# Performance work log

Hardware: AMD Instinct MI355X
Metric: run time of the kernel (lower is better)

## Reference

```python
import jax, jax.numpy as jnp
import numpy as np

NUM_BINS = 32
SIGMA_RATIO = 1.0
SMOOTH_NR = 1e-7
SMOOTH_DR = 1e-7


def _parzen_weights(x, bin_centers, preterm):
    # x: [B, N]; returns normalized Gaussian Parzen weights [B, N, K]
    d = x[..., None] - bin_centers  # [B, N, K]
    w = jnp.exp(-preterm * d * d)
    return w / jnp.sum(w, axis=-1, keepdims=True)


def _mi_loss(pred, target):
    B = pred.shape[0]
    p = pred.reshape(B, -1)  # [B, N]
    t = target.reshape(B, -1)
    N = p.shape[1]

    # min/max are detached (.item() in torch); images in [0,1] use fixed range (0,1)
    minval = jax.lax.stop_gradient(jnp.minimum(p.min(), t.min()))
    maxval = jax.lax.stop_gradient(jnp.maximum(p.max(), t.max()))
    in_range = (maxval <= 1.0) & (minval >= 0.0)
    minval = jnp.where(in_range, jnp.float32(0.0), minval)
    maxval = jnp.where(in_range, jnp.float32(1.0), maxval)

    bin_centers = minval + (maxval - minval) * jnp.linspace(0.0, 1.0, NUM_BINS, dtype=p.dtype)  # [K]
    sigma = (maxval - minval) / (NUM_BINS - 1) * SIGMA_RATIO
    preterm = 1.0 / (2.0 * sigma * sigma)

    wa = _parzen_weights(p, bin_centers, preterm)  # [B, N, K]
    wb = _parzen_weights(t, bin_centers, preterm)  # [B, N, K]

    pa = jnp.mean(wa, axis=1)  # [B, K] == pa of shape B,1,K squeezed
    pb = jnp.mean(wb, axis=1)  # [B, K]
    pab = jnp.einsum('bnk,bnl->bkl', wa, wb) / N  # [B, K, K] joint histogram
    papb = pa[:, :, None] * pb[:, None, :]  # [B, K, K] outer product == bmm(pa^T, pb)

    mi = jnp.sum(pab * jnp.log((pab + SMOOTH_NR) / (papb + SMOOTH_DR) + SMOOTH_DR), axis=(-1, -2))  # [B]
    return -jnp.mean(mi)  # reduction='mean', negated


def setup_inputs() -> dict:
    key = jax.random.key(0)
    k1, k2 = jax.random.split(key)
    shape = (1, 1, 128, 128, 128)
    pred = jax.random.uniform(k1, shape, dtype=jnp.float32)
    target = jax.random.uniform(k2, shape, dtype=jnp.float32)
    return {"pred": pred, "target": target}


def reference(pred, target):
    return _mi_loss(pred, target)
```

## Files before the change

### kernel.cpp

```cpp
#include <hip/hip_runtime.h>
#include <math.h>

#ifndef __has_builtin
#define __has_builtin(x) 0
#endif
#if __has_builtin(__builtin_amdgcn_exp2f)
#define EXP2F(x) __builtin_amdgcn_exp2f(x)
#else
#define EXP2F(x) exp2f(x)
#endif
#if __has_builtin(__builtin_amdgcn_rcpf)
#define RCPF(x) __builtin_amdgcn_rcpf(x)
#else
#define RCPF(x) (1.0f / (x))
#endif

typedef _Float16 f16x8 __attribute__((ext_vector_type(8)));
typedef _Float16 h2 __attribute__((ext_vector_type(2)));
typedef float f32x4 __attribute__((ext_vector_type(4)));

union Frag {
  f16x8 v;
  h2 p[4];
  _Float16 e[8];
};

__device__ __forceinline__ h2 pkrtz(float a, float b) {
#if __has_builtin(__builtin_amdgcn_cvt_pkrtz)
  return __builtin_bit_cast(h2, __builtin_amdgcn_cvt_pkrtz(a, b));
#else
  h2 r; r.x = (_Float16)a; r.y = (_Float16)b; return r;
#endif
}

constexpr int KBINS = 32;
constexpr int MM_BLOCKS = 512;
constexpr int MAIN_BLOCKS = 1024;
constexpr int NTHR = 512;
constexpr int WPB = 8;
constexpr int BATCH = 32;
constexpr int RED_BLOCKS = 64;
constexpr int PART_OFF_F = 4096;
constexpr size_t REDA_OFF_B = (size_t)(PART_OFF_F + MAIN_BLOCKS * KBINS * KBINS) * 4;
constexpr float WSCALE = 512.0f;

#define MFMA16(a, b, c) __builtin_amdgcn_mfma_f32_16x16x32_f16((a), (b), (c), 0, 0, 0)

template <int CTRL>
__device__ __forceinline__ float rot_add(float v) {
  int r = __builtin_amdgcn_update_dpp(0, __builtin_bit_cast(int, v), CTRL, 0xF, 0xF, true);
  return v + __builtin_bit_cast(float, r);
}
__device__ __forceinline__ float row_sum16(float v) {
  v = rot_add<0x128>(v);
  v = rot_add<0x124>(v);
  v = rot_add<0x122>(v);
  v = rot_add<0x121>(v);
  return v;
}

__device__ __forceinline__ void wpair(float x, float c0, float c1, float npl2,
                                      float& w0, float& w1) {
  float d0 = x - c0, d1 = x - c1;
  float e0 = EXP2F(fmaf(npl2 * d0, d0, 9.0f));
  float e1 = EXP2F(fmaf(npl2 * d1, d1, 9.0f));
  float s = row_sum16(e0 + e1);
  float inv = RCPF(s);
  inv = inv * fmaf(-s, inv, 2.0f);
  inv *= WSCALE;
  w0 = e0 * inv;
  w1 = e1 * inv;
}

__global__ __launch_bounds__(256) void k_minmax(const float* __restrict__ p,
                                                const float* __restrict__ t,
                                                int n, float* __restrict__ ws) {
  int tid = blockIdx.x * 256 + threadIdx.x;
  int nth = gridDim.x * 256;
  float mn = INFINITY, mx = -INFINITY;
  int n4 = n >> 2;
  const float4* p4 = (const float4*)p;
  const float4* t4 = (const float4*)t;
  for (int i = tid; i < n4; i += nth) {
    float4 a = p4[i];
    mn = fminf(mn, fminf(fminf(a.x, a.y), fminf(a.z, a.w)));
    mx = fmaxf(mx, fmaxf(fmaxf(a.x, a.y), fmaxf(a.z, a.w)));
    float4 b = t4[i];
    mn = fminf(mn, fminf(fminf(b.x, b.y), fminf(b.z, b.w)));
    mx = fmaxf(mx, fmaxf(fmaxf(b.x, b.y), fmaxf(b.z, b.w)));
  }
  for (int i = (n4 << 2) + tid; i < n; i += nth) {
    mn = fminf(mn, fminf(p[i], t[i]));
    mx = fmaxf(mx, fmaxf(p[i], t[i]));
  }
  for (int off = 32; off; off >>= 1) {
    mn = fminf(mn, __shfl_xor(mn, off, 64));
    mx = fmaxf(mx, __shfl_xor(mx, off, 64));
  }
  __shared__ float smn[4], smx[4];
  int wv = threadIdx.x >> 6;
  if ((threadIdx.x & 63) == 0) { smn[wv] = mn; smx[wv] = mx; }
  __syncthreads();
  if (threadIdx.x == 0) {
    mn = fminf(fminf(smn[0], smn[1]), fminf(smn[2], smn[3]));
    mx = fmaxf(fmaxf(smx[0], smx[1]), fmaxf(smx[2], smx[3]));
    ws[16 + 2 * blockIdx.x] = mn;
    ws[17 + 2 * blockIdx.x] = mx;
  }
}

__global__ __launch_bounds__(NTHR, 4) void k_main(const float* __restrict__ p,
                                                  const float* __restrict__ t,
                                                  int n, float* __restrict__ ws) {
  __shared__ __align__(16) float red[WPB][KBINS * KBINS];
  __shared__ float s_par[4];

  const int tidx = threadIdx.x;
  const int lane = tidx & 63;
  const int wv = tidx >> 6;

  if (tidx < 64) {
    float mn = INFINITY, mx = -INFINITY;
    for (int b = lane; b < MM_BLOCKS; b += 64) {
      mn = fminf(mn, ws[16 + 2 * b]);
      mx = fmaxf(mx, ws[17 + 2 * b]);
    }
    for (int off = 32; off; off >>= 1) {
      mn = fminf(mn, __shfl_xor(mn, off, 64));
      mx = fmaxf(mx, __shfl_xor(mx, off, 64));
    }
    if (lane == 0) {
      bool in_range = (mx <= 1.0f) && (mn >= 0.0f);
      float minv = in_range ? 0.0f : mn;
      float maxv = in_range ? 1.0f : mx;
      float drange = maxv - minv;
      float sigma = drange * (1.0f / (KBINS - 1));
      float preterm = 1.0f / (2.0f * sigma * sigma);
      s_par[0] = minv;
      s_par[1] = drange * (1.0f / (KBINS - 1));
      s_par[2] = preterm * 1.44269504088896340736f;
    }
  }
  __syncthreads();
  const float minv = s_par[0], delta = s_par[1];
  const float npl2 = -s_par[2];

  const int m = lane & 15;
  const int quad = lane >> 4;
  const int qb = quad << 3;
  const float c0 = fmaf(delta, (float)m, minv);
  const float c1 = fmaf(delta, (float)(m + 16), minv);

  f32x4 acc00 = {0.f, 0.f, 0.f, 0.f};
  f32x4 acc01 = {0.f, 0.f, 0.f, 0.f};
  f32x4 acc10 = {0.f, 0.f, 0.f, 0.f};
  f32x4 acc11 = {0.f, 0.f, 0.f, 0.f};

  const int per_wave = n >> 13;
  const int base = (blockIdx.x * WPB + wv) * per_wave;

  for (int it = 0; it < per_wave; it += BATCH) {
    const int sbase = base + it + qb;
    float4 a0 = *(const float4*)(p + sbase);
    float4 a1 = *(const float4*)(p + sbase + 4);
    float4 b0 = *(const float4*)(t + sbase);
    float4 b1 = *(const float4*)(t + sbase + 4);
    float xa[8] = {a0.x, a0.y, a0.z, a0.w, a1.x, a1.y, a1.z, a1.w};
    float xb[8] = {b0.x, b0.y, b0.z, b0.w, b1.x, b1.y, b1.z, b1.w};

    Frag Ah0, Al0, Ah1, Al1, Bh0, Bl0, Bh1, Bl1;
#pragma unroll
    for (int jp = 0; jp < 4; ++jp) {
      {
        float w00, w10, w01, w11;
        wpair(xa[2 * jp], c0, c1, npl2, w00, w10);
        wpair(xa[2 * jp + 1], c0, c1, npl2, w01, w11);
        h2 h0 = pkrtz(w00, w01);
        h2 h1 = pkrtz(w10, w11);
        Ah0.p[jp] = h0;
        Ah1.p[jp] = h1;
        Al0.p[jp] = pkrtz(w00 - (float)h0.x, w01 - (float)h0.y);
        Al1.p[jp] = pkrtz(w10 - (float)h1.x, w11 - (float)h1.y);
      }
      {
        float w00, w10, w01, w11;
        wpair(xb[2 * jp], c0, c1, npl2, w00, w10);
        wpair(xb[2 * jp + 1], c0, c1, npl2, w01, w11);
        h2 h0 = pkrtz(w00, w01);
        h2 h1 = pkrtz(w10, w11);
        Bh0.p[jp] = h0;
        Bh1.p[jp] = h1;
        Bl0.p[jp] = pkrtz(w00 - (float)h0.x, w01 - (float)h0.y);
        Bl1.p[jp] = pkrtz(w10 - (float)h1.x, w11 - (float)h1.y);
      }
    }
    acc00 = MFMA16(Ah0.v, Bh0.v, acc00);
    acc01 = MFMA16(Ah0.v, Bh1.v, acc01);
    acc10 = MFMA16(Ah1.v, Bh0.v, acc10);
    acc11 = MFMA16(Ah1.v, Bh1.v, acc11);
    acc00 = MFMA16(Al0.v, Bh0.v, acc00);
    acc01 = MFMA16(Al0.v, Bh1.v, acc01);
    acc10 = MFMA16(Al1.v, Bh0.v, acc10);
    acc11 = MFMA16(Al1.v, Bh1.v, acc11);
    acc00 = MFMA16(Ah0.v, Bl0.v, acc00);
    acc01 = MFMA16(Ah0.v, Bl1.v, acc01);
    acc10 = MFMA16(Ah1.v, Bl0.v, acc10);
    acc11 = MFMA16(Ah1.v, Bl1.v, acc11);
    acc00 = MFMA16(Al0.v, Bl0.v, acc00);
    acc01 = MFMA16(Al0.v, Bl1.v, acc01);
    acc10 = MFMA16(Al1.v, Bl0.v, acc10);
    acc11 = MFMA16(Al1.v, Bl1.v, acc11);
  }

#pragma unroll
  for (int reg = 0; reg < 4; ++reg) {
    int r0 = quad * 4 + reg;
    red[wv][r0 * KBINS + m] = acc00[reg];
    red[wv][r0 * KBINS + 16 + m] = acc01[reg];
    red[wv][(16 + r0) * KBINS + m] = acc10[reg];
    red[wv][(16 + r0) * KBINS + 16 + m] = acc11[reg];
  }
  __syncthreads();
  {
    int c = 2 * tidx;
    float s0 = 0.f, s1 = 0.f;
#pragma unroll
    for (int w = 0; w < WPB; ++w) {
      float2 v = *(const float2*)&red[w][c];
      s0 += v.x;
      s1 += v.y;
    }
    *(float2*)(ws + PART_OFF_F + (size_t)blockIdx.x * 1024 + c) = make_float2(s0, s1);
  }
}

__global__ __launch_bounds__(1024) void k_reduceA(float* __restrict__ ws) {
  const float* part = ws + PART_OFF_F;
  double* outp = (double*)((char*)ws + REDA_OFF_B);
  int tid = threadIdx.x;
  int r = blockIdx.x;
  double s = 0.0;
#pragma unroll
  for (int b = 0; b < MAIN_BLOCKS / RED_BLOCKS; ++b)
    s += (double)part[(size_t)(r * (MAIN_BLOCKS / RED_BLOCKS) + b) * 1024 + tid];
  outp[(size_t)r * 1024 + tid] = s;
}

__global__ __launch_bounds__(1024) void k_final(const float* __restrict__ ws_f,
                                                float* __restrict__ out, int n) {
  const double* parts = (const double*)((const char*)ws_f + REDA_OFF_B);
  __shared__ double pab_s[1024];
  __shared__ double pa_s[32], pb_s[32];
  __shared__ double wsum[16];
  int tid = threadIdx.x;
  double s = 0.0;
#pragma unroll 8
  for (int r = 0; r < RED_BLOCKS; ++r) s += parts[(size_t)r * 1024 + tid];
  double pab = s / ((double)n * 262144.0);
  pab_s[tid] = pab;
  __syncthreads();
  if (tid < 32) {
    double a = 0.0;
    for (int l = 0; l < 32; ++l) a += pab_s[tid * 32 + l];
    pa_s[tid] = a;
  } else if (tid < 64) {
    int l = tid - 32;
    double b = 0.0;
    for (int k2 = 0; k2 < 32; ++k2) b += pab_s[k2 * 32 + l];
    pb_s[l] = b;
  }
  __syncthreads();
  int k = tid >> 5, l = tid & 31;
  double papb = pa_s[k] * pb_s[l];
  double v = pab * log((pab + 1e-7) / (papb + 1e-7) + 1e-7);
  for (int off = 32; off; off >>= 1) v += __shfl_down(v, off, 64);
  if ((tid & 63) == 0) wsum[tid >> 6] = v;
  __syncthreads();
  if (tid < 64) {
    double w = (tid < 16) ? wsum[tid] : 0.0;
    for (int off = 8; off; off >>= 1) w += __shfl_down(w, off, 64);
    if (tid == 0) out[0] = (float)(-w);
  }
}

extern "C" void kernel_launch(void* const* d_in, const int* in_sizes, int n_in,
                              void* d_out, int out_size, void* d_ws, size_t ws_size,
                              hipStream_t stream) {
  const float* p = (const float*)d_in[0];
  const float* t = (const float*)d_in[1];
  float* out = (float*)d_out;
  float* ws = (float*)d_ws;
  int n = in_sizes[0];

  k_minmax<<<dim3(MM_BLOCKS), dim3(256), 0, stream>>>(p, t, n, ws);
  k_main<<<dim3(MAIN_BLOCKS), dim3(NTHR), 0, stream>>>(p, t, n, ws);
  k_reduceA<<<dim3(RED_BLOCKS), dim3(1024), 0, stream>>>(ws);
  k_final<<<dim3(1), dim3(1024), 0, stream>>>(ws, out, n);
}
```

Measured before the change: 130.2 us.

## Fold Parzen normalization into one weight side and replace reduce kernel with atomics

Computes raw Gaussian exponentials for both inputs and applies a single combined reciprocal of the product of row sums to the pred-side weights, leaving target weights only scaled. This halves reciprocal/normalization work in the VALU-heavy main loop. The separate partial-reduction kernel is removed; blocks instead atomically add double partials into 8 slots zeroed by the minmax kernel, saving a launch at the cost of atomic contention and nondeterministic summation order. The removed exp bias changes fp16 dynamic range, which risks some precision loss.

```diff
diff --git a/kernel.cpp b/kernel.cpp
--- a/kernel.cpp
+++ b/kernel.cpp
@@ -39,10 +39,8 @@
 constexpr int NTHR = 512;
 constexpr int WPB = 8;
 constexpr int BATCH = 32;
-constexpr int RED_BLOCKS = 64;
-constexpr int PART_OFF_F = 4096;
-constexpr size_t REDA_OFF_B = (size_t)(PART_OFF_F + MAIN_BLOCKS * KBINS * KBINS) * 4;
-constexpr float WSCALE = 512.0f;
+constexpr int NSLOT = 8;
+constexpr int ACC_OFF_F = 4096;
 
 #define MFMA16(a, b, c) __builtin_amdgcn_mfma_f32_16x16x32_f16((a), (b), (c), 0, 0, 0)
 
@@ -59,17 +57,12 @@
   return v;
 }
 
-__device__ __forceinline__ void wpair(float x, float c0, float c1, float npl2,
-                                      float& w0, float& w1) {
+__device__ __forceinline__ void eraw(float x, float c0, float c1, float npl2,
+                                     float& e0, float& e1, float& s) {
   float d0 = x - c0, d1 = x - c1;
-  float e0 = EXP2F(fmaf(npl2 * d0, d0, 9.0f));
-  float e1 = EXP2F(fmaf(npl2 * d1, d1, 9.0f));
-  float s = row_sum16(e0 + e1);
-  float inv = RCPF(s);
-  inv = inv * fmaf(-s, inv, 2.0f);
-  inv *= WSCALE;
-  w0 = e0 * inv;
-  w1 = e1 * inv;
+  e0 = EXP2F((npl2 * d0) * d0);
+  e1 = EXP2F((npl2 * d1) * d1);
+  s = row_sum16(e0 + e1);
 }
 
 __global__ __launch_bounds__(256) void k_minmax(const float* __restrict__ p,
@@ -77,6 +70,8 @@
                                                 int n, float* __restrict__ ws) {
   int tid = blockIdx.x * 256 + threadIdx.x;
   int nth = gridDim.x * 256;
+  if (tid < NSLOT * 1024) ((double*)(ws + ACC_OFF_F))[tid] = 0.0;
+
   float mn = INFINITY, mx = -INFINITY;
   int n4 = n >> 2;
   const float4* p4 = (const float4*)p;
@@ -171,28 +166,38 @@
     Frag Ah0, Al0, Ah1, Al1, Bh0, Bl0, Bh1, Bl1;
 #pragma unroll
     for (int jp = 0; jp < 4; ++jp) {
-      {
-        float w00, w10, w01, w11;
-        wpair(xa[2 * jp], c0, c1, npl2, w00, w10);
-        wpair(xa[2 * jp + 1], c0, c1, npl2, w01, w11);
-        h2 h0 = pkrtz(w00, w01);
-        h2 h1 = pkrtz(w10, w11);
-        Ah0.p[jp] = h0;
-        Ah1.p[jp] = h1;
-        Al0.p[jp] = pkrtz(w00 - (float)h0.x, w01 - (float)h0.y);
-        Al1.p[jp] = pkrtz(w10 - (float)h1.x, w11 - (float)h1.y);
-      }
-      {
-        float w00, w10, w01, w11;
-        wpair(xb[2 * jp], c0, c1, npl2, w00, w10);
-        wpair(xb[2 * jp + 1], c0, c1, npl2, w01, w11);
-        h2 h0 = pkrtz(w00, w01);
-        h2 h1 = pkrtz(w10, w11);
-        Bh0.p[jp] = h0;
-        Bh1.p[jp] = h1;
-        Bl0.p[jp] = pkrtz(w00 - (float)h0.x, w01 - (float)h0.y);
-        Bl1.p[jp] = pkrtz(w10 - (float)h1.x, w11 - (float)h1.y);
-      }
+      float ea00, ea01, sa0, ea10, ea11, sa1;
+      float eb00, eb01, sb0, eb10, eb11, sb1;
+      eraw(xa[2 * jp],     c0, c1, npl2, ea00, ea01, sa0);
+      eraw(xa[2 * jp + 1], c0, c1, npl2, ea10, ea11, sa1);
+      eraw(xb[2 * jp],     c0, c1, npl2, eb00, eb01, sb0);
+      eraw(xb[2 * jp + 1], c0, c1, npl2, eb10, eb11, sb1);
+      float pr0 = sa0 * sb0;
+      float i0 = RCPF(pr0);
+      i0 = i0 * fmaf(-pr0, i0, 2.0f);
+      i0 *= 4096.0f;
+      float pr1 = sa1 * sb1;
+      float i1 = RCPF(pr1);
+      i1 = i1 * fmaf(-pr1, i1, 2.0f);
+      i1 *= 4096.0f;
+      float wa00 = ea00 * i0, wa01 = ea01 * i0;
+      float wa10 = ea10 * i1, wa11 = ea11 * i1;
+      float wb00 = eb00 * 64.0f, wb01 = eb01 * 64.0f;
+      float wb10 = eb10 * 64.0f, wb11 = eb11 * 64.0f;
+      h2 ha0 = pkrtz(wa00, wa10);
+      h2 ha1 = pkrtz(wa01, wa11);
+      h2 hb0 = pkrtz(wb00, wb10);
+      h2 hb1 = pkrtz(wb01, wb11);
+      Ah0.p[jp] = ha0; Ah1.p[jp] = ha1;
+      Bh0.p[jp] = hb0; Bh1.p[jp] = hb1;
+      Al0.e[2 * jp]     = (_Float16)(wa00 - (float)ha0.x);
+      Al0.e[2 * jp + 1] = (_Float16)(wa10 - (float)ha0.y);
+      Al1.e[2 * jp]     = (_Float16)(wa01 - (float)ha1.x);
+      Al1.e[2 * jp + 1] = (_Float16)(wa11 - (float)ha1.y);
+      Bl0.e[2 * jp]     = (_Float16)(wb00 - (float)hb0.x);
+      Bl0.e[2 * jp + 1] = (_Float16)(wb10 - (float)hb0.y);
+      Bl1.e[2 * jp]     = (_Float16)(wb01 - (float)hb1.x);
+      Bl1.e[2 * jp + 1] = (_Float16)(wb11 - (float)hb1.y);
     }
     acc00 = MFMA16(Ah0.v, Bh0.v, acc00);
     acc01 = MFMA16(Ah0.v, Bh1.v, acc01);
@@ -230,32 +235,22 @@
       s0 += v.x;
       s1 += v.y;
     }
-    *(float2*)(ws + PART_OFF_F + (size_t)blockIdx.x * 1024 + c) = make_float2(s0, s1);
-  }
-}
-
-__global__ __launch_bounds__(1024) void k_reduceA(float* __restrict__ ws) {
-  const float* part = ws + PART_OFF_F;
-  double* outp = (double*)((char*)ws + REDA_OFF_B);
-  int tid = threadIdx.x;
-  int r = blockIdx.x;
-  double s = 0.0;
-#pragma unroll
-  for (int b = 0; b < MAIN_BLOCKS / RED_BLOCKS; ++b)
-    s += (double)part[(size_t)(r * (MAIN_BLOCKS / RED_BLOCKS) + b) * 1024 + tid];
-  outp[(size_t)r * 1024 + tid] = s;
+    double* acc = (double*)(ws + ACC_OFF_F) + (size_t)(blockIdx.x & (NSLOT - 1)) * 1024;
+    unsafeAtomicAdd(&acc[c], (double)s0);
+    unsafeAtomicAdd(&acc[c + 1], (double)s1);
+  }
 }
 
 __global__ __launch_bounds__(1024) void k_final(const float* __restrict__ ws_f,
                                                 float* __restrict__ out, int n) {
-  const double* parts = (const double*)((const char*)ws_f + REDA_OFF_B);
+  const double* acc = (const double*)(ws_f + ACC_OFF_F);
   __shared__ double pab_s[1024];
   __shared__ double pa_s[32], pb_s[32];
   __shared__ double wsum[16];
   int tid = threadIdx.x;
   double s = 0.0;
-#pragma unroll 8
-  for (int r = 0; r < RED_BLOCKS; ++r) s += parts[(size_t)r * 1024 + tid];
+#pragma unroll
+  for (int slot = 0; slot < NSLOT; ++slot) s += acc[(size_t)slot * 1024 + tid];
   double pab = s / ((double)n * 262144.0);
   pab_s[tid] = pab;
   __syncthreads();
@@ -294,6 +289,5 @@
 
   k_minmax<<<dim3(MM_BLOCKS), dim3(256), 0, stream>>>(p, t, n, ws);
   k_main<<<dim3(MAIN_BLOCKS), dim3(NTHR), 0, stream>>>(p, t, n, ws);
-  k_reduceA<<<dim3(RED_BLOCKS), dim3(1024), 0, stream>>>(ws);
   k_final<<<dim3(1), dim3(1024), 0, stream>>>(ws, out, n);
 }
```

After: 128.6 us. Within noise of the previous version (-1.2%).
